# Kernel tuning notes

Measured on AMD Instinct MI355X. Metric: run time of the kernel, lower is better.

Reference implementation:

```python
import jax, jax.numpy as jnp
import numpy as np

D_MODEL = 768
D_STATE = 64
D_CONV = 4
D_INNER = 1536          # expand * d_model
HEADDIM = 64
NHEADS = D_INNER // HEADDIM  # 24
RANK = 8
SCALE = 16.0 / RANK     # lora alpha / rank = 2.0
D_IN_PROJ = 2 * D_INNER + 2 * D_STATE + NHEADS  # 3224
CONV_DIM = D_INNER + 2 * D_STATE                # 1664
EPS = 1e-6


def _rmsnorm(x, w):
    return x * jax.lax.rsqrt(jnp.mean(x * x, axis=-1, keepdims=True) + EPS) * w


def _loop_rope(x, loop_index):
    # per-loop-index RoPE: same rotation applied to every token/position
    inv_freq = 1.0 / (10000.0 ** (jnp.arange(0, D_MODEL, 2, dtype=jnp.float32) / D_MODEL))
    freqs = jnp.float32(loop_index) * inv_freq
    cos_v = jnp.repeat(jnp.cos(freqs), 2)[:D_MODEL].astype(x.dtype)
    sin_v = jnp.repeat(jnp.sin(freqs), 2)[:D_MODEL].astype(x.dtype)
    rot = jnp.stack([-x[..., 1::2], x[..., ::2]], axis=-1).reshape(x.shape)
    return x * cos_v + rot * sin_v


def _mamba2_core(x, in_base, lora_A_in, lora_B_in, conv_w, conv_b, dt_bias,
                 A_log, D_param, gated_norm_w, out_base, lora_A_out, lora_B_out):
    Bsz, L, _ = x.shape
    # LoRA-adapted input projection
    W_in = in_base + SCALE * (lora_B_in @ lora_A_in)          # (3224, 768)
    zxbcdt = x @ W_in.T                                       # (b, l, 3224)
    z = zxbcdt[..., :D_INNER]                                 # gate branch
    xBC = zxbcdt[..., D_INNER:D_INNER + CONV_DIM]             # conv branch
    dt = jax.nn.softplus(zxbcdt[..., -NHEADS:] + dt_bias)     # (b, l, h)
    # depthwise causal conv1d + silu
    xc = jax.lax.conv_general_dilated(
        xBC.transpose(0, 2, 1), conv_w[:, None, :], (1,), [(D_CONV - 1, 0)],
        dimension_numbers=('NCH', 'OIH', 'NCH'), feature_group_count=CONV_DIM)
    xBC = jax.nn.silu(xc.transpose(0, 2, 1) + conv_b)
    xs = xBC[..., :D_INNER].reshape(Bsz, L, NHEADS, HEADDIM)  # (b, l, h, p)
    Bm = xBC[..., D_INNER:D_INNER + D_STATE]                  # (b, l, n)
    Cm = xBC[..., D_INNER + D_STATE:]                         # (b, l, n)
    A = -jnp.exp(A_log)                                       # (h,)
    dA = jnp.exp(dt * A)                                      # (b, l, h)
    # sequential selective scan (same math as chunked SSD)
    def step(h, inp):
        dA_t, dt_t, B_t, C_t, x_t = inp
        h = dA_t[:, :, None, None] * h + jnp.einsum('bh,bn,bhp->bhpn', dt_t, B_t, x_t)
        y = jnp.einsum('bn,bhpn->bhp', C_t, h)
        return h, y
    tm = lambda a: jnp.moveaxis(a, 1, 0)  # time-major
    h0 = jnp.zeros((Bsz, NHEADS, HEADDIM, D_STATE), x.dtype)
    _, y = jax.lax.scan(step, h0, (tm(dA), tm(dt), tm(Bm), tm(Cm), tm(xs)))
    y = jnp.moveaxis(y, 0, 1) + D_param[None, None, :, None] * xs  # skip term
    y = y.reshape(Bsz, L, D_INNER)
    # gated RMSNorm (RMSNormGated): norm(y * silu(z))
    y = _rmsnorm(y * jax.nn.silu(z), gated_norm_w)
    # LoRA-adapted output projection
    W_out = out_base + SCALE * (lora_B_out @ lora_A_out)      # (768, 1536)
    return y @ W_out.T


def _forward(x, x_prompt, in_base, lora_A_in, lora_B_in, conv_w, conv_b, dt_bias,
             A_log, D_param, gated_norm_w, out_base, lora_A_out, lora_B_out,
             loop_norm_w, lifeline_gate, n_loops):
    for i in range(n_loops):
        h = _loop_rope(_rmsnorm(x, loop_norm_w), i)
        h = _mamba2_core(h, in_base, lora_A_in, lora_B_in, conv_w, conv_b, dt_bias,
                         A_log, D_param, gated_norm_w, out_base, lora_A_out, lora_B_out)
        x = h + lifeline_gate * x_prompt   # lifeline gated residual injection
    return x


def setup_inputs() -> dict:
    key = jax.random.key(0)
    ks = jax.random.split(key, 12)
    f32 = jnp.float32
    rn = lambda k, s, sc=0.02: jax.random.normal(k, s, dtype=f32) * sc
    return {
        'x': jax.random.normal(ks[0], (2, 1024, D_MODEL), f32),
        'x_prompt': jax.random.normal(ks[1], (2, 1024, D_MODEL), f32),
        'in_base': rn(ks[2], (D_IN_PROJ, D_MODEL)),
        'lora_A_in': rn(ks[3], (RANK, D_MODEL), 0.1),
        'lora_B_in': rn(ks[4], (D_IN_PROJ, RANK), 0.01),
        'conv_w': rn(ks[5], (CONV_DIM, D_CONV), 0.1),
        'conv_b': jnp.zeros((CONV_DIM,), f32),
        'dt_bias': rn(ks[6], (NHEADS,), 0.5),
        'A_log': jnp.log(jnp.linspace(1.0, 16.0, NHEADS, dtype=f32)),
        'D_param': jnp.ones((NHEADS,), f32),
        'gated_norm_w': jnp.ones((D_INNER,), f32),
        'out_base': rn(ks[7], (D_MODEL, D_INNER)),
        'lora_A_out': rn(ks[8], (RANK, D_INNER), 0.1),
        'lora_B_out': rn(ks[9], (D_MODEL, RANK), 0.01),
        'loop_norm_w': jnp.ones((D_MODEL,), f32),
        'lifeline_gate': jnp.ones((D_MODEL,), f32),
        'n_loops': 2,
    }


def reference(x, x_prompt, in_base, lora_A_in, lora_B_in, conv_w, conv_b, dt_bias,
              A_log, D_param, gated_norm_w, out_base, lora_A_out, lora_B_out,
              loop_norm_w, lifeline_gate, n_loops):
    return _forward(x, x_prompt, in_base, lora_A_in, lora_B_in, conv_w, conv_b, dt_bias,
                    A_log, D_param, gated_norm_w, out_base, lora_A_out, lora_B_out,
                    loop_norm_w, lifeline_gate, n_loops)
```

## Files before the change

### kernel.cpp

```cpp
#include <hip/hip_runtime.h>
#include <hip/hip_bf16.h>
#include <math.h>

#define D_MODEL 768
#define D_STATE 64
#define D_CONV 4
#define D_INNER 1536
#define HEADDIM 64
#define NHEADS 24
#define RANK 8
#define D_IN_PROJ 3224
#define NPAD 3328
#define ZSTR 3328
#define CONV_DIM 1664
#define BSZ 2
#define SEQ 1024
#define NROWS (BSZ*SEQ)
#define SCALE_LORA 2.0f
#define LC 64
#define NCHUNK (SEQ/LC)
#define LSTR 72

typedef __attribute__((ext_vector_type(8))) short bf16x8;
typedef __attribute__((ext_vector_type(4))) float f32x4;


__device__ inline float waveReduceSum(float v) {
#pragma unroll
    for (int m = 32; m; m >>= 1) v += __shfl_xor(v, m, 64);
    return v;
}

template <int NWAVES>
__device__ inline float blockReduceSum(float v) {
    __shared__ float tmp[NWAVES];
    int lane = threadIdx.x & 63, wid = threadIdx.x >> 6;
    v = waveReduceSum(v);
    if (lane == 0) tmp[wid] = v;
    __syncthreads();
    float tot = 0.f;
#pragma unroll
    for (int i = 0; i < NWAVES; i++) tot += tmp[i];
    return tot;
}

__device__ inline float sigmoidf_(float x) { return 1.f / (1.f + expf(-x)); }

__device__ inline unsigned short f2bf(float f) {
    union { float f; unsigned int u; } v; v.f = f;
    unsigned int r = (v.u + 0x7fffu + ((v.u >> 16) & 1u)) >> 16;
    return (unsigned short)r;
}

__device__ inline void load_lds16(const void* g, void* l) {
    __builtin_amdgcn_global_load_lds((const __attribute__((address_space(1))) void*)g,
                                     (__attribute__((address_space(3))) void*)l, 16, 0, 0);
}


__global__ void build_w_in_kernel(const float* __restrict__ base,
                                  const float* __restrict__ lA,
                                  const float* __restrict__ lB,
                                  unsigned short* __restrict__ W) {
    int idx = blockIdx.x * blockDim.x + threadIdx.x;
    if (idx >= NPAD * D_MODEL) return;
    int r = idx / D_MODEL, c = idx - r * D_MODEL;
    if (r >= D_IN_PROJ) { W[idx] = 0; return; }
    float s = 0.f;
#pragma unroll
    for (int k = 0; k < RANK; k++) s += lB[r * RANK + k] * lA[k * D_MODEL + c];
    W[idx] = f2bf(base[(size_t)r * D_MODEL + c] + SCALE_LORA * s);
}

__global__ void build_w_out_kernel(const float* __restrict__ base,
                                   const float* __restrict__ lA,
                                   const float* __restrict__ lB,
                                   unsigned short* __restrict__ W) {
    int idx = blockIdx.x * blockDim.x + threadIdx.x;
    if (idx >= D_MODEL * D_INNER) return;
    int r = idx / D_INNER, c = idx - r * D_INNER;
    float s = 0.f;
#pragma unroll
    for (int k = 0; k < RANK; k++) s += lB[r * RANK + k] * lA[k * D_INNER + c];
    W[idx] = f2bf(base[idx] + SCALE_LORA * s);
}

__global__ __launch_bounds__(384) void rmsrope_kernel(
    const float* __restrict__ x, const float* __restrict__ w,
    unsigned short* __restrict__ out, int loop_i) {
    int row = blockIdx.x;
    const float* xr = x + (size_t)row * D_MODEL;
    int j = threadIdx.x;
    float x0 = xr[2 * j], x1 = xr[2 * j + 1];
    float ss = blockReduceSum<6>(x0 * x0 + x1 * x1);
    float sc = rsqrtf(ss * (1.f / D_MODEL) + 1e-6f);
    float y0 = x0 * sc * w[2 * j];
    float y1 = x1 * sc * w[2 * j + 1];
    float ang = (float)loop_i * expf((float)(2 * j) * (-9.210340371976184f / (float)D_MODEL));
    float c = cosf(ang), sn = sinf(ang);
    unsigned short* orow = out + (size_t)row * D_MODEL;
    orow[2 * j]     = f2bf(y0 * c - y1 * sn);
    orow[2 * j + 1] = f2bf(y1 * c + y0 * sn);
}

__global__ __launch_bounds__(256) void gemm_pipe_kernel(
    const unsigned short* __restrict__ A,
    const unsigned short* __restrict__ B,
    float* __restrict__ C, int M, int N, int K, int Cstride,
    int Ks, int mode) {
    __shared__ unsigned short lsA[2][128 * 64];
    __shared__ unsigned short lsB[2][128 * 64];
    int t = threadIdx.x;
    int w = t >> 6, lane = t & 63;
    int n0 = blockIdx.x * 128, m0 = blockIdx.y * 128;
    int kbase = blockIdx.z * Ks;
    int wr = w >> 1, wc = w & 1;
    f32x4 acc[4][4];
#pragma unroll
    for (int i = 0; i < 4; i++)
#pragma unroll
        for (int j = 0; j < 4; j++) acc[i][j] = (f32x4){0.f, 0.f, 0.f, 0.f};

#define STAGE(bi, kk0)                                                           \
    {                                                                            \
        _Pragma("unroll")                                                        \
        for (int o = 0; o < 4; o++) {                                            \
            int s = o * 256 + t;                                                 \
            int row = s >> 3, u = s & 7;                                         \
            int usrc = (u ^ (row & 7)) << 3;                                     \
            unsigned short* la = &lsA[bi][(size_t)(o * 256 + (t & ~63)) * 8];    \
            unsigned short* lb = &lsB[bi][(size_t)(o * 256 + (t & ~63)) * 8];    \
            load_lds16(&A[(size_t)(m0 + row) * K + (kk0) + usrc], la);           \
            load_lds16(&B[(size_t)(n0 + row) * K + (kk0) + usrc], lb);           \
        }                                                                        \
    }

    int nk = Ks >> 6;
    STAGE(0, kbase);
    __syncthreads();
    int cur = 0;
    for (int ks = 0; ks < nk; ks++) {
        if (ks + 1 < nk) STAGE(cur ^ 1, kbase + (ks + 1) * 64);
#pragma unroll
        for (int kk = 0; kk < 2; kk++) {
            bf16x8 af[4], bfr[4];
            int u_t = kk * 4 + (lane >> 4);
            int kof = (u_t ^ (lane & 7)) << 3;
#pragma unroll
            for (int i = 0; i < 4; i++) {
                int row = wr * 64 + i * 16 + (lane & 15);
                af[i] = *(const bf16x8*)&lsA[cur][row * 64 + kof];
            }
#pragma unroll
            for (int j = 0; j < 4; j++) {
                int row = wc * 64 + j * 16 + (lane & 15);
                bfr[j] = *(const bf16x8*)&lsB[cur][row * 64 + kof];
            }
#pragma unroll
            for (int i = 0; i < 4; i++)
#pragma unroll
                for (int j = 0; j < 4; j++)
                    acc[i][j] = __builtin_amdgcn_mfma_f32_16x16x32_bf16(af[i], bfr[j], acc[i][j], 0, 0, 0);
        }
        __syncthreads();
        cur ^= 1;
    }
#undef STAGE

#pragma unroll
    for (int i = 0; i < 4; i++) {
#pragma unroll
        for (int j = 0; j < 4; j++) {
#pragma unroll
            for (int r = 0; r < 4; r++) {
                int row = m0 + wr * 64 + i * 16 + (lane >> 4) * 4 + r;
                int col = n0 + wc * 64 + j * 16 + (lane & 15);
                float v = acc[i][j][r];
                if (mode) atomicAdd(&C[(size_t)row * Cstride + col], v);
                else      C[(size_t)row * Cstride + col] = v;
            }
        }
    }
}

__global__ void epilog_init_kernel(const float* __restrict__ xp,
                                   const float* __restrict__ gate,
                                   float* __restrict__ out) {
    int idx = blockIdx.x * blockDim.x + threadIdx.x;
    if (idx >= NROWS * D_MODEL / 4) return;
    float4 xv = ((const float4*)xp)[idx];
    int n0 = (idx * 4) % D_MODEL;
    float4 g = *(const float4*)&gate[n0];
    float4 o = make_float4(g.x * xv.x, g.y * xv.y, g.z * xv.z, g.w * xv.w);
    ((float4*)out)[idx] = o;
}

__global__ void conv_kernel(const float* __restrict__ zx, const float* __restrict__ cw,
                            const float* __restrict__ cb, float* __restrict__ xbc) {
    int idx = blockIdx.x * blockDim.x + threadIdx.x;
    if (idx >= BSZ * SEQ * CONV_DIM) return;
    int c = idx % CONV_DIM;
    int l = (idx / CONV_DIM) % SEQ;
    int b = idx / (CONV_DIM * SEQ);
    const float* base = zx + (size_t)b * SEQ * ZSTR + D_INNER + c;
    float acc = cb[c];
#pragma unroll
    for (int t = 0; t < 4; t++) {
        int ll = l - 3 + t;
        if (ll >= 0) acc = fmaf(cw[c * 4 + t], base[(size_t)ll * ZSTR], acc);
    }
    xbc[idx] = acc * sigmoidf_(acc);
}

__global__ __launch_bounds__(256) void scan_mfma_kernel(
    const float* __restrict__ xbc,
    const float* __restrict__ zx,
    const float* __restrict__ dt_bias,
    const float* __restrict__ A_log,
    const float* __restrict__ Dp,
    float* __restrict__ y,
    float* __restrict__ Fbuf,
    float* __restrict__ cumA) {
    __shared__ unsigned short Cc[64][LSTR];
    __shared__ unsigned short Bb[64][LSTR];
    __shared__ unsigned short Xt[64][LSTR];
    __shared__ unsigned short Bw[64][LSTR];
    __shared__ unsigned short Mm[64][LSTR];
    __shared__ float s_lds[64];
    __shared__ float dt_lds[64];

    int blk = blockIdx.x;
    int c = blk % NCHUNK;
    int bh = blk / NCHUNK;
    int h = bh % NHEADS, b = bh / NHEADS;
    int tid = threadIdx.x;
    int w = tid >> 6, lane = tid & 63;
    const int t0 = c * LC;

    if (w == 0) {
        int t = lane;
        size_t row = (size_t)(b * SEQ + t0 + t);
        float raw = zx[row * ZSTR + (D_INNER + CONV_DIM) + h] + dt_bias[h];
        float dt_t = raw > 20.f ? raw : log1pf(expf(raw));
        float s = dt_t * (-expf(A_log[h]));
#pragma unroll
        for (int off = 1; off < 64; off <<= 1) {
            float v = __shfl_up(s, off, 64);
            if (lane >= off) s += v;
        }
        s_lds[t] = s;
        dt_lds[t] = dt_t;
        cumA[(size_t)blk * LC + t] = expf(s);
    }

    float breg[16];
#pragma unroll
    for (int k = 0; k < 16; k++) {
        int idx = k * 256 + tid;
        int r = idx >> 6, ci = idx & 63;
        size_t row = (size_t)(b * SEQ + t0 + r) * CONV_DIM;
        float cv = xbc[row + D_INNER + D_STATE + ci];
        float bv = xbc[row + D_INNER + ci];
        float xv = xbc[row + h * HEADDIM + ci];
        Cc[r][ci] = f2bf(cv);
        Bb[r][ci] = f2bf(bv);
        Xt[ci][r] = f2bf(xv);
        breg[k] = bv;
    }
    __syncthreads();

    float s63 = s_lds[63];
#pragma unroll
    for (int k = 0; k < 16; k++) {
        int idx = k * 256 + tid;
        int r = idx >> 6, ci = idx & 63;
        float wu = expf(s63 - s_lds[r]) * dt_lds[r];
        Bw[ci][r] = f2bf(breg[k] * wu);
    }

    f32x4 accG[4];
#pragma unroll
    for (int j = 0; j < 4; j++) accG[j] = (f32x4){0.f, 0.f, 0.f, 0.f};
#pragma unroll
    for (int kk = 0; kk < 2; kk++) {
        int kof = kk * 32 + (lane >> 4) * 8;
        bf16x8 afr = *(const bf16x8*)&Cc[16 * w + (lane & 15)][kof];
#pragma unroll
        for (int j = 0; j < 4; j++) {
            bf16x8 bfr = *(const bf16x8*)&Bb[16 * j + (lane & 15)][kof];
            accG[j] = __builtin_amdgcn_mfma_f32_16x16x32_bf16(afr, bfr, accG[j], 0, 0, 0);
        }
    }
#pragma unroll
    for (int j = 0; j < 4; j++) {
#pragma unroll
        for (int r = 0; r < 4; r++) {
            int t = 16 * w + (lane >> 4) * 4 + r;
            int u = 16 * j + (lane & 15);
            float v = 0.f;
            if (u <= t) v = accG[j][r] * dt_lds[u] * expf(s_lds[t] - s_lds[u]);
            Mm[t][u] = f2bf(v);
        }
    }
    __syncthreads();

    f32x4 accY[4];
#pragma unroll
    for (int j = 0; j < 4; j++) accY[j] = (f32x4){0.f, 0.f, 0.f, 0.f};
#pragma unroll
    for (int kk = 0; kk < 2; kk++) {
        int kof = kk * 32 + (lane >> 4) * 8;
        bf16x8 afr = *(const bf16x8*)&Mm[16 * w + (lane & 15)][kof];
#pragma unroll
        for (int j = 0; j < 4; j++) {
            bf16x8 bfr = *(const bf16x8*)&Xt[16 * j + (lane & 15)][kof];
            accY[j] = __builtin_amdgcn_mfma_f32_16x16x32_bf16(afr, bfr, accY[j], 0, 0, 0);
        }
    }
    float D_h = Dp[h];
#pragma unroll
    for (int j = 0; j < 4; j++) {
#pragma unroll
        for (int r = 0; r < 4; r++) {
            int t = 16 * w + (lane >> 4) * 4 + r;
            int p = 16 * j + (lane & 15);
            size_t row = (size_t)(b * SEQ + t0 + t);
            float xv = xbc[row * CONV_DIM + h * HEADDIM + p];
            y[row * D_INNER + h * HEADDIM + p] = accY[j][r] + D_h * xv;
        }
    }

    f32x4 accF[4];
#pragma unroll
    for (int j = 0; j < 4; j++) accF[j] = (f32x4){0.f, 0.f, 0.f, 0.f};
#pragma unroll
    for (int kk = 0; kk < 2; kk++) {
        int kof = kk * 32 + (lane >> 4) * 8;
        bf16x8 afr = *(const bf16x8*)&Bw[16 * w + (lane & 15)][kof];
#pragma unroll
        for (int j = 0; j < 4; j++) {
            bf16x8 bfr = *(const bf16x8*)&Xt[16 * j + (lane & 15)][kof];
            accF[j] = __builtin_amdgcn_mfma_f32_16x16x32_bf16(afr, bfr, accF[j], 0, 0, 0);
        }
    }
#pragma unroll
    for (int j = 0; j < 4; j++) {
#pragma unroll
        for (int r = 0; r < 4; r++) {
            int n = 16 * w + (lane >> 4) * 4 + r;
            int p = 16 * j + (lane & 15);
            Fbuf[(size_t)blk * (HEADDIM * D_STATE) + n * HEADDIM + p] = accF[j][r];
        }
    }
}

__global__ __launch_bounds__(256) void combine_kernel(
    const float* __restrict__ Fbuf, const float* __restrict__ cumA,
    float* __restrict__ Hinit) {
    int bh = blockIdx.x >> 4;
    int np = (blockIdx.x & 15) * 256 + threadIdx.x;
    float H = 0.f;
#pragma unroll
    for (int c = 0; c < NCHUNK; c++) {
        size_t idx = (size_t)(bh * NCHUNK + c) * (HEADDIM * D_STATE) + np;
        float pA = cumA[(size_t)(bh * NCHUNK + c) * LC + (LC - 1)];
        Hinit[idx] = H;
        H = fmaf(pA, H, Fbuf[idx]);
    }
}

__global__ __launch_bounds__(256) void ycorr_kernel(
    const float* __restrict__ xbc, const float* __restrict__ cumA,
    const float* __restrict__ Hinit, float* __restrict__ y) {
    int blk = blockIdx.x;
    int c = blk % NCHUNK;
    int bh = blk / NCHUNK;
    int h = bh % NHEADS, b = bh / NHEADS;
    __shared__ float Cd[LC][D_STATE + 1];
    __shared__ float Hs[D_STATE][HEADDIM + 1];
    int tid = threadIdx.x;
    size_t cbase = (size_t)blk * LC;
    size_t hbase = (size_t)blk * (HEADDIM * D_STATE);
#pragma unroll
    for (int k = 0; k < 16; k++) {
        int idx = tid + k * 256;
        int r = idx >> 6, n = idx & 63;
        size_t row = (size_t)(b * SEQ + c * LC + r);
        Cd[r][n] = xbc[row * CONV_DIM + D_INNER + D_STATE + n] * cumA[cbase + r];
        Hs[r][n] = Hinit[hbase + idx];
    }
    __syncthreads();
    int tx = tid & 15, ty = tid >> 4;
    float acc[4][4] = {};
    for (int n = 0; n < D_STATE; n++) {
        float cv[4], hv[4];
#pragma unroll
        for (int i = 0; i < 4; i++) cv[i] = Cd[ty * 4 + i][n];
#pragma unroll
        for (int j = 0; j < 4; j++) hv[j] = Hs[n][tx * 4 + j];
#pragma unroll
        for (int i = 0; i < 4; i++)
#pragma unroll
            for (int j = 0; j < 4; j++)
                acc[i][j] = fmaf(cv[i], hv[j], acc[i][j]);
    }
#pragma unroll
    for (int i = 0; i < 4; i++) {
        int tt = ty * 4 + i;
        size_t row = (size_t)(b * SEQ + c * LC + tt);
#pragma unroll
        for (int j = 0; j < 4; j++) {
            int p = tx * 4 + j;
            size_t oidx = row * D_INNER + h * HEADDIM + p;
            y[oidx] += acc[i][j];
        }
    }
}

__global__ __launch_bounds__(256) void gatenorm_kernel(
    const float* __restrict__ y, const float* __restrict__ zx,
    const float* __restrict__ w, unsigned short* __restrict__ out) {
    int row = blockIdx.x;
    const float* z = zx + (size_t)row * ZSTR;
    const float* yr = y + (size_t)row * D_INNER;
    float g[6];
    float ss = 0.f;
#pragma unroll
    for (int e = 0; e < 6; e++) {
        int idx = threadIdx.x + e * 256;
        float zv = z[idx];
        float gv = yr[idx] * (zv * sigmoidf_(zv));
        g[e] = gv;
        ss += gv * gv;
    }
    ss = blockReduceSum<4>(ss);
    float sc = rsqrtf(ss * (1.f / D_INNER) + 1e-6f);
#pragma unroll
    for (int e = 0; e < 6; e++) {
        int idx = threadIdx.x + e * 256;
        out[(size_t)row * D_INNER + idx] = f2bf(g[e] * sc * w[idx]);
    }
}

extern "C" void kernel_launch(void* const* d_in, const int* in_sizes, int n_in,
                              void* d_out, int out_size, void* d_ws, size_t ws_size,
                              hipStream_t stream) {
    const float* x        = (const float*)d_in[0];
    const float* x_prompt = (const float*)d_in[1];
    const float* in_base  = (const float*)d_in[2];
    const float* lA_in    = (const float*)d_in[3];
    const float* lB_in    = (const float*)d_in[4];
    const float* conv_w   = (const float*)d_in[5];
    const float* conv_b   = (const float*)d_in[6];
    const float* dt_bias  = (const float*)d_in[7];
    const float* A_log    = (const float*)d_in[8];
    const float* D_param  = (const float*)d_in[9];
    const float* gnw      = (const float*)d_in[10];
    const float* out_base = (const float*)d_in[11];
    const float* lA_out   = (const float*)d_in[12];
    const float* lB_out   = (const float*)d_in[13];
    const float* loop_nw  = (const float*)d_in[14];
    const float* gate     = (const float*)d_in[15];
    float* out = (float*)d_out;

    float* ws_f = (float*)d_ws;
    float* zx    = ws_f;
    float* xbc   = zx    + (size_t)NROWS * ZSTR;
    float* ybuf  = xbc   + (size_t)NROWS * CONV_DIM;
    float* Fbuf  = ybuf  + (size_t)NROWS * D_INNER;
    float* Hinit = Fbuf  + (size_t)BSZ * NHEADS * NCHUNK * HEADDIM * D_STATE;
    float* cumA  = Hinit + (size_t)BSZ * NHEADS * NCHUNK * HEADDIM * D_STATE;
    unsigned short* W_in  = (unsigned short*)(cumA + (size_t)BSZ * NHEADS * NCHUNK * LC);
    unsigned short* W_out = W_in  + (size_t)NPAD * D_MODEL;
    unsigned short* hbuf  = W_out + (size_t)D_MODEL * D_INNER;
    unsigned short* ygt   = hbuf  + (size_t)NROWS * D_MODEL;

    build_w_in_kernel<<<(NPAD * D_MODEL + 255) / 256, 256, 0, stream>>>(in_base, lA_in, lB_in, W_in);
    build_w_out_kernel<<<(D_MODEL * D_INNER + 255) / 256, 256, 0, stream>>>(out_base, lA_out, lB_out, W_out);

    for (int i = 0; i < 2; i++) {
        const float* xsrc = (i == 0) ? x : out;
        rmsrope_kernel<<<NROWS, 384, 0, stream>>>(xsrc, loop_nw, hbuf, i);

        dim3 g1(NPAD / 128, NROWS / 128, 1);
        gemm_pipe_kernel<<<g1, 256, 0, stream>>>(hbuf, W_in, zx, NROWS, NPAD, D_MODEL, ZSTR,
                                                 D_MODEL, 0);

        conv_kernel<<<(BSZ * SEQ * CONV_DIM + 255) / 256, 256, 0, stream>>>(zx, conv_w, conv_b, xbc);

        scan_mfma_kernel<<<BSZ * NHEADS * NCHUNK, 256, 0, stream>>>(
            xbc, zx, dt_bias, A_log, D_param, ybuf, Fbuf, cumA);
        combine_kernel<<<BSZ * NHEADS * 16, 256, 0, stream>>>(Fbuf, cumA, Hinit);
        ycorr_kernel<<<BSZ * NHEADS * NCHUNK, 256, 0, stream>>>(xbc, cumA, Hinit, ybuf);

        gatenorm_kernel<<<NROWS, 256, 0, stream>>>(ybuf, zx, gnw, ygt);

        epilog_init_kernel<<<(NROWS * D_MODEL / 4 + 255) / 256, 256, 0, stream>>>(x_prompt, gate, out);
        dim3 g2(D_MODEL / 128, NROWS / 128, 4);
        gemm_pipe_kernel<<<g2, 256, 0, stream>>>(ygt, W_out, out, NROWS, D_MODEL, D_INNER, D_MODEL,
                                                 D_INNER / 4, 1);
    }
}
```

Before: 327.7 us.

## Store in-projection output as bf16 and fuse x-conv into scan

The input-projection GEMM now writes its output as bf16 instead of fp32, and writes the dt columns separately in fp32. The depthwise conv for the x channels moves into the scan kernel's load phase, so a separate conv pass only produces the small B/C buffer. The D-skip term reuses the conv output already held in LDS, and the x_prompt*gate output init is folded into the gatenorm kernel. Together these aim to cut global memory traffic and one kernel launch per loop. The cost is bf16 rounding of z and the conv inputs, plus the conv being recomputed inside each scan block.

```diff
diff --git a/kernel.cpp b/kernel.cpp
--- a/kernel.cpp
+++ b/kernel.cpp
@@ -51,6 +51,9 @@
     unsigned int r = (v.u + 0x7fffu + ((v.u >> 16) & 1u)) >> 16;
     return (unsigned short)r;
 }
+__device__ inline float bf2f(unsigned short u) {
+    union { unsigned int i; float f; } v; v.i = ((unsigned int)u) << 16; return v.f;
+}
 
 __device__ inline void load_lds16(const void* g, void* l) {
     __builtin_amdgcn_global_load_lds((const __attribute__((address_space(1))) void*)g,
@@ -103,11 +106,12 @@
     orow[2 * j + 1] = f2bf(y1 * c + y0 * sn);
 }
 
+template <int MODE>
 __global__ __launch_bounds__(256) void gemm_pipe_kernel(
     const unsigned short* __restrict__ A,
     const unsigned short* __restrict__ B,
-    float* __restrict__ C, int M, int N, int K, int Cstride,
-    int Ks, int mode) {
+    void* __restrict__ Cv, int M, int N, int K, int Cstride,
+    int Ks, float* __restrict__ dtraw) {
     __shared__ unsigned short lsA[2][128 * 64];
     __shared__ unsigned short lsB[2][128 * 64];
     int t = threadIdx.x;
@@ -176,45 +180,41 @@
                 int row = m0 + wr * 64 + i * 16 + (lane >> 4) * 4 + r;
                 int col = n0 + wc * 64 + j * 16 + (lane & 15);
                 float v = acc[i][j][r];
-                if (mode) atomicAdd(&C[(size_t)row * Cstride + col], v);
-                else      C[(size_t)row * Cstride + col] = v;
+                if (MODE == 1) {
+                    atomicAdd(&((float*)Cv)[(size_t)row * Cstride + col], v);
+                } else {
+                    ((unsigned short*)Cv)[(size_t)row * Cstride + col] = f2bf(v);
+                    if (col >= 3200 && col < 3224) dtraw[row * 24 + (col - 3200)] = v;
+                }
             }
         }
     }
 }
 
-__global__ void epilog_init_kernel(const float* __restrict__ xp,
-                                   const float* __restrict__ gate,
-                                   float* __restrict__ out) {
+__global__ void conv_bc_kernel(const unsigned short* __restrict__ zxb,
+                               const float* __restrict__ cw,
+                               const float* __restrict__ cb, float* __restrict__ xbc) {
     int idx = blockIdx.x * blockDim.x + threadIdx.x;
-    if (idx >= NROWS * D_MODEL / 4) return;
-    float4 xv = ((const float4*)xp)[idx];
-    int n0 = (idx * 4) % D_MODEL;
-    float4 g = *(const float4*)&gate[n0];
-    float4 o = make_float4(g.x * xv.x, g.y * xv.y, g.z * xv.z, g.w * xv.w);
-    ((float4*)out)[idx] = o;
-}
-
-__global__ void conv_kernel(const float* __restrict__ zx, const float* __restrict__ cw,
-                            const float* __restrict__ cb, float* __restrict__ xbc) {
-    int idx = blockIdx.x * blockDim.x + threadIdx.x;
-    if (idx >= BSZ * SEQ * CONV_DIM) return;
-    int c = idx % CONV_DIM;
-    int l = (idx / CONV_DIM) % SEQ;
-    int b = idx / (CONV_DIM * SEQ);
-    const float* base = zx + (size_t)b * SEQ * ZSTR + D_INNER + c;
-    float acc = cb[c];
+    if (idx >= NROWS * 128) return;
+    int cbc = idx & 127;
+    int row = idx >> 7;
+    int l = row & (SEQ - 1);
+    int ch = 1536 + cbc;
+    const unsigned short* base = zxb + (size_t)row * ZSTR + 3072 + cbc;
+    float acc = cb[ch];
 #pragma unroll
     for (int t = 0; t < 4; t++) {
         int ll = l - 3 + t;
-        if (ll >= 0) acc = fmaf(cw[c * 4 + t], base[(size_t)ll * ZSTR], acc);
+        if (ll >= 0) acc = fmaf(cw[ch * 4 + t], bf2f(base[(size_t)(ll - l) * ZSTR]), acc);
     }
     xbc[idx] = acc * sigmoidf_(acc);
 }
 
 __global__ __launch_bounds__(256) void scan_mfma_kernel(
+    const unsigned short* __restrict__ zxb,
     const float* __restrict__ xbc,
-    const float* __restrict__ zx,
+    const float* __restrict__ dtraw,
+    const float* __restrict__ cw, const float* __restrict__ cb,
     const float* __restrict__ dt_bias,
     const float* __restrict__ A_log,
     const float* __restrict__ Dp,
@@ -240,7 +240,7 @@
     if (w == 0) {
         int t = lane;
         size_t row = (size_t)(b * SEQ + t0 + t);
-        float raw = zx[row * ZSTR + (D_INNER + CONV_DIM) + h] + dt_bias[h];
+        float raw = dtraw[row * 24 + h] + dt_bias[h];
         float dt_t = raw > 20.f ? raw : log1pf(expf(raw));
         float s = dt_t * (-expf(A_log[h]));
 #pragma unroll
@@ -258,13 +258,22 @@
     for (int k = 0; k < 16; k++) {
         int idx = k * 256 + tid;
         int r = idx >> 6, ci = idx & 63;
-        size_t row = (size_t)(b * SEQ + t0 + r) * CONV_DIM;
-        float cv = xbc[row + D_INNER + D_STATE + ci];
-        float bv = xbc[row + D_INNER + ci];
-        float xv = xbc[row + h * HEADDIM + ci];
+        int l = t0 + r;
+        size_t grow = (size_t)(b * SEQ + l);
+        int ch = h * 64 + ci;
+        float accv = cb[ch];
+        const unsigned short* xin = zxb + grow * ZSTR + 1536 + ch;
+#pragma unroll
+        for (int tap = 0; tap < 4; tap++) {
+            int ll = l - 3 + tap;
+            if (ll >= 0) accv = fmaf(cw[ch * 4 + tap], bf2f(xin[(size_t)(tap - 3) * ZSTR]), accv);
+        }
+        float xv = accv * sigmoidf_(accv);
+        Xt[ci][r] = f2bf(xv);
+        float bv = xbc[grow * 128 + ci];
+        float cv = xbc[grow * 128 + 64 + ci];
         Cc[r][ci] = f2bf(cv);
         Bb[r][ci] = f2bf(bv);
-        Xt[ci][r] = f2bf(xv);
         breg[k] = bv;
     }
     __syncthreads();
@@ -325,7 +334,7 @@
             int t = 16 * w + (lane >> 4) * 4 + r;
             int p = 16 * j + (lane & 15);
             size_t row = (size_t)(b * SEQ + t0 + t);
-            float xv = xbc[row * CONV_DIM + h * HEADDIM + p];
+            float xv = bf2f(Xt[p][t]);
             y[row * D_INNER + h * HEADDIM + p] = accY[j][r] + D_h * xv;
         }
     }
@@ -386,7 +395,7 @@
         int idx = tid + k * 256;
         int r = idx >> 6, n = idx & 63;
         size_t row = (size_t)(b * SEQ + c * LC + r);
-        Cd[r][n] = xbc[row * CONV_DIM + D_INNER + D_STATE + n] * cumA[cbase + r];
+        Cd[r][n] = xbc[row * 128 + 64 + n] * cumA[cbase + r];
         Hs[r][n] = Hinit[hbase + idx];
     }
     __syncthreads();
@@ -418,17 +427,19 @@
 }
 
 __global__ __launch_bounds__(256) void gatenorm_kernel(
-    const float* __restrict__ y, const float* __restrict__ zx,
-    const float* __restrict__ w, unsigned short* __restrict__ out) {
+    const float* __restrict__ y, const unsigned short* __restrict__ zxb,
+    const float* __restrict__ w, unsigned short* __restrict__ out,
+    const float* __restrict__ xp, const float* __restrict__ gate,
+    float* __restrict__ outbuf) {
     int row = blockIdx.x;
-    const float* z = zx + (size_t)row * ZSTR;
+    const unsigned short* z = zxb + (size_t)row * ZSTR;
     const float* yr = y + (size_t)row * D_INNER;
     float g[6];
     float ss = 0.f;
 #pragma unroll
     for (int e = 0; e < 6; e++) {
         int idx = threadIdx.x + e * 256;
-        float zv = z[idx];
+        float zv = bf2f(z[idx]);
         float gv = yr[idx] * (zv * sigmoidf_(zv));
         g[e] = gv;
         ss += gv * gv;
@@ -439,6 +450,13 @@
     for (int e = 0; e < 6; e++) {
         int idx = threadIdx.x + e * 256;
         out[(size_t)row * D_INNER + idx] = f2bf(g[e] * sc * w[idx]);
+    }
+    if (threadIdx.x < 192) {
+        int q = threadIdx.x;
+        float4 xv4 = ((const float4*)(xp + (size_t)row * D_MODEL))[q];
+        float4 g4 = ((const float4*)gate)[q];
+        ((float4*)(outbuf + (size_t)row * D_MODEL))[q] =
+            make_float4(g4.x * xv4.x, g4.y * xv4.y, g4.z * xv4.z, g4.w * xv4.w);
     }
 }
 
@@ -464,13 +482,14 @@
     float* out = (float*)d_out;
 
     float* ws_f = (float*)d_ws;
-    float* zx    = ws_f;
-    float* xbc   = zx    + (size_t)NROWS * ZSTR;
-    float* ybuf  = xbc   + (size_t)NROWS * CONV_DIM;
+    float* dtraw = ws_f;
+    float* xbc   = dtraw + (size_t)NROWS * 24;
+    float* ybuf  = xbc   + (size_t)NROWS * 128;
     float* Fbuf  = ybuf  + (size_t)NROWS * D_INNER;
     float* Hinit = Fbuf  + (size_t)BSZ * NHEADS * NCHUNK * HEADDIM * D_STATE;
     float* cumA  = Hinit + (size_t)BSZ * NHEADS * NCHUNK * HEADDIM * D_STATE;
-    unsigned short* W_in  = (unsigned short*)(cumA + (size_t)BSZ * NHEADS * NCHUNK * LC);
+    unsigned short* zxb   = (unsigned short*)(cumA + (size_t)BSZ * NHEADS * NCHUNK * LC);
+    unsigned short* W_in  = zxb   + (size_t)NROWS * ZSTR;
     unsigned short* W_out = W_in  + (size_t)NPAD * D_MODEL;
     unsigned short* hbuf  = W_out + (size_t)D_MODEL * D_INNER;
     unsigned short* ygt   = hbuf  + (size_t)NROWS * D_MODEL;
@@ -483,21 +502,20 @@
         rmsrope_kernel<<<NROWS, 384, 0, stream>>>(xsrc, loop_nw, hbuf, i);
 
         dim3 g1(NPAD / 128, NROWS / 128, 1);
-        gemm_pipe_kernel<<<g1, 256, 0, stream>>>(hbuf, W_in, zx, NROWS, NPAD, D_MODEL, ZSTR,
-                                                 D_MODEL, 0);
-
-        conv_kernel<<<(BSZ * SEQ * CONV_DIM + 255) / 256, 256, 0, stream>>>(zx, conv_w, conv_b, xbc);
+        gemm_pipe_kernel<2><<<g1, 256, 0, stream>>>(hbuf, W_in, zxb, NROWS, NPAD, D_MODEL, ZSTR,
+                                                    D_MODEL, dtraw);
+
+        conv_bc_kernel<<<(NROWS * 128 + 255) / 256, 256, 0, stream>>>(zxb, conv_w, conv_b, xbc);
 
         scan_mfma_kernel<<<BSZ * NHEADS * NCHUNK, 256, 0, stream>>>(
-            xbc, zx, dt_bias, A_log, D_param, ybuf, Fbuf, cumA);
+            zxb, xbc, dtraw, conv_w, conv_b, dt_bias, A_log, D_param, ybuf, Fbuf, cumA);
         combine_kernel<<<BSZ * NHEADS * 16, 256, 0, stream>>>(Fbuf, cumA, Hinit);
         ycorr_kernel<<<BSZ * NHEADS * NCHUNK, 256, 0, stream>>>(xbc, cumA, Hinit, ybuf);
 
-        gatenorm_kernel<<<NROWS, 256, 0, stream>>>(ybuf, zx, gnw, ygt);
-
-        epilog_init_kernel<<<(NROWS * D_MODEL / 4 + 255) / 256, 256, 0, stream>>>(x_prompt, gate, out);
+        gatenorm_kernel<<<NROWS, 256, 0, stream>>>(ybuf, zxb, gnw, ygt, x_prompt, gate, out);
+
         dim3 g2(D_MODEL / 128, NROWS / 128, 4);
-        gemm_pipe_kernel<<<g2, 256, 0, stream>>>(ygt, W_out, out, NROWS, D_MODEL, D_INNER, D_MODEL,
-                                                 D_INNER / 4, 1);
-    }
-}
+        gemm_pipe_kernel<1><<<g2, 256, 0, stream>>>(ygt, W_out, out, NROWS, D_MODEL, D_INNER, D_MODEL,
+                                                    D_INNER / 4, nullptr);
+    }
+}
```

Result: no change. 330.1 us (+0.7%).
